# Kernel tuning notes

Measured on AMD Instinct MI355X. Metric: run time of the kernel, lower is better.

Reference implementation:

```python
import jax, jax.numpy as jnp
import numpy as np

S, T, B = 32, 64, 64          # sentences, tokens/sentence, batch
V, E, H, G, C = 32000, 128, 128, 128, 5  # vocab, embed, intra hid, inter hid, classes


def _gru_dir(x, h0, Wih, Whh, bih, bhh):
    # x: [T,B,D]; Wih: [3H,D]; Whh: [3H,H]  (PyTorch GRU gate order r,z,n)
    xg = jnp.einsum('tbd,gd->tbg', x, Wih) + bih  # precompute input gates [T,B,3H]
    def step(h, xt):
        gh = h @ Whh.T + bhh
        ir, iz, inn = jnp.split(xt, 3, axis=-1)
        hr, hz, hn = jnp.split(gh, 3, axis=-1)
        r = jax.nn.sigmoid(ir + hr)
        z = jax.nn.sigmoid(iz + hz)
        n = jnp.tanh(inn + r * hn)
        hnew = (1 - z) * n + z * h
        return hnew, hnew
    _, out = jax.lax.scan(step, h0, xg)
    return out  # [T,B,H]


def _bigru(x, Wih, Whh, bih, bhh):
    # x: [T,B,D]; Wih: [2,3H,D] (fwd, bwd). Zero initial state (init_hidden()).
    h0 = jnp.zeros((x.shape[1], Whh.shape[-1]), x.dtype)
    of = _gru_dir(x, h0, Wih[0], Whh[0], bih[0], bhh[0])
    ob = _gru_dir(x[::-1], h0, Wih[1], Whh[1], bih[1], bhh[1])[::-1]
    return jnp.concatenate([of, ob], axis=-1)  # [T,B,2H]


def setup_inputs() -> dict:
    key = jax.random.key(0)
    ks = iter(jax.random.split(key, 20))
    u = lambda k, shp, s: jax.random.uniform(k, shp, jnp.float32, -s, s)
    tokens = jax.random.randint(next(ks), (S, T, B), 0, V)
    return {
        'tokens': tokens,
        'embed_table': jax.random.normal(next(ks), (V, E), jnp.float32),
        # intra biGRU (input E, hidden H)
        'Wih_intra': u(next(ks), (2, 3 * H, E), 0.08),
        'Whh_intra': u(next(ks), (2, 3 * H, H), 0.08),
        'bih_intra': u(next(ks), (2, 3 * H), 0.08),
        'bhh_intra': u(next(ks), (2, 3 * H), 0.08),
        # intra attention
        'W_W_intra': u(next(ks), (2 * H, 2 * H), 0.1),
        'b_intra': u(next(ks), (2 * H,), 0.1),
        'proj_intra': u(next(ks), (2 * H,), 0.1),
        # inter biGRU (input 2H, hidden G)
        'Wih_inter': u(next(ks), (2, 3 * G, 2 * H), 0.08),
        'Whh_inter': u(next(ks), (2, 3 * G, G), 0.08),
        'bih_inter': u(next(ks), (2, 3 * G), 0.08),
        'bhh_inter': u(next(ks), (2, 3 * G), 0.08),
        # inter attention
        'W_W_inter': u(next(ks), (2 * G, 2 * G), 0.1),
        'b_inter': u(next(ks), (2 * G,), 0.1),
        'proj_inter': u(next(ks), (2 * G,), 0.1),
        # final linear
        'W_final': u(next(ks), (C, 2 * G), 0.06),
        'b_final': u(next(ks), (C,), 0.06),
    }


def reference(tokens, embed_table, Wih_intra, Whh_intra, bih_intra, bhh_intra,
              W_W_intra, b_intra, proj_intra, Wih_inter, Whh_inter, bih_inter,
              bhh_inter, W_W_inter, b_inter, proj_inter, W_final, b_final):
    # ---- intra (word-level) per sentence, fresh zero state each sentence ----
    emb = embed_table[tokens]                                   # [S,T,B,E]
    intra_out = jax.vmap(
        lambda xs: _bigru(xs, Wih_intra, Whh_intra, bih_intra, bhh_intra)
    )(emb)                                                      # [S,T,B,2H]
    u1 = jnp.tanh(jnp.einsum('stbh,hk->stbk', intra_out, W_W_intra) + b_intra)
    a1 = jnp.einsum('stbk,k->stb', u1, proj_intra)              # [S,T,B]
    a1 = jax.nn.softmax(a1, axis=1)                             # softmax over tokens
    sent_vecs = jnp.einsum('stb,stbh->sbh', a1, intra_out)      # [S,B,2H]
    # ---- inter (sentence-level) ----
    inter_out = _bigru(sent_vecs, Wih_inter, Whh_inter, bih_inter, bhh_inter)  # [S,B,2G]
    u2 = jnp.tanh(jnp.einsum('sbh,hk->sbk', inter_out, W_W_inter) + b_inter)
    a2 = jnp.einsum('sbk,k->sb', u2, proj_inter)                # NO softmax (faithful to source)
    doc_vec = jnp.einsum('sb,sbh->bh', a2, inter_out)           # [B,2G]
    final_map = doc_vec @ W_final.T + b_final                   # [B,C]
    return final_map
```

## Files before the change

kernel.cpp:

```cpp
#include <hip/hip_runtime.h>

#define S_ 32
#define T_ 64
#define B_ 64
#define V_ 32000
#define E_ 128
#define H_ 128
#define G_ 128
#define C_ 5

typedef short s8v __attribute__((ext_vector_type(8)));
typedef __bf16 b8v __attribute__((ext_vector_type(8)));
typedef float f32x4 __attribute__((ext_vector_type(4)));

template <typename V>
__device__ inline auto mfma_sel(V a, V b, f32x4 c, int)
    -> decltype(__builtin_amdgcn_mfma_f32_16x16x32_bf16(a, b, c, 0, 0, 0)) {
  return __builtin_amdgcn_mfma_f32_16x16x32_bf16(a, b, c, 0, 0, 0);
}
template <typename V>
__device__ inline f32x4 mfma_sel(V a, V b, f32x4 c, long) {
  return __builtin_amdgcn_mfma_f32_16x16x32_bf16(
      __builtin_bit_cast(b8v, a), __builtin_bit_cast(b8v, b), c, 0, 0, 0);
}
__device__ inline f32x4 mfma16(s8v a, s8v b, f32x4 c) { return mfma_sel(a, b, c, 0); }

__device__ inline float b2f(unsigned short u) {
  union { unsigned int i; float f; } v; v.i = ((unsigned int)u) << 16; return v.f;
}
__device__ inline unsigned short f2b(float f) {
  union { float f; unsigned int i; } v; v.f = f;
  return (unsigned short)((v.i + 0x8000u) >> 16);
}
__device__ inline unsigned short f2b_rne(float f) {
  union { float f; unsigned int i; } v; v.f = f;
  unsigned int r = (v.i + 0x7fffu + ((v.i >> 16) & 1u)) >> 16;
  return (unsigned short)r;
}
__device__ inline s8v cvt8(const float* p) {
  const float4 a = *(const float4*)p;
  const float4 b = *(const float4*)(p + 4);
  s8v r;
  r[0] = (short)f2b_rne(a.x); r[1] = (short)f2b_rne(a.y);
  r[2] = (short)f2b_rne(a.z); r[3] = (short)f2b_rne(a.w);
  r[4] = (short)f2b_rne(b.x); r[5] = (short)f2b_rne(b.y);
  r[6] = (short)f2b_rne(b.z); r[7] = (short)f2b_rne(b.w);
  return r;
}
__device__ inline float fsigm(float x) {
  return __builtin_amdgcn_rcpf(1.f + __builtin_amdgcn_exp2f(-1.44269504f * x));
}
__device__ inline float ftanh(float x) {
  return 1.f - 2.f * __builtin_amdgcn_rcpf(1.f + __builtin_amdgcn_exp2f(2.88539008f * x));
}

__device__ inline void lds_barrier() {
  asm volatile("s_waitcnt lgkmcnt(0)\n\ts_barrier" ::: "memory");
}

__global__ __launch_bounds__(256) void k_gtab(
    const float* __restrict__ emb,
    const float* __restrict__ wih,
    const float* __restrict__ bih,
    const float* __restrict__ bhh,
    const float* __restrict__ wwi,
    const float* __restrict__ wihI,
    unsigned short* __restrict__ gtab,
    unsigned short* __restrict__ wta,
    unsigned short* __restrict__ wib)
{
  __shared__ __align__(16) unsigned short res[64 * 776];
  __shared__ __align__(16) unsigned short alds[64 * 136];
  const int bid = blockIdx.x, tid = threadIdx.x;
  if (bid >= 504) {
    const int cb = bid - 504;
    for (int i = 0; i < 48; ++i) {
      int e4 = cb * 12288 + i * 256 + tid;
      float4 v = *(const float4*)&wihI[(size_t)e4 * 4];
      ushort4 u;
      u.x = f2b_rne(v.x); u.y = f2b_rne(v.y); u.z = f2b_rne(v.z); u.w = f2b_rne(v.w);
      *(ushort4*)&wib[(size_t)e4 * 4] = u;
    }
    return;
  }
  if (bid >= 500) {
    const int n0 = (bid - 500) * 64;
    for (int i = 0; i < 64; ++i) {
      int cid = i * 256 + tid;
      int k = cid >> 6, nl = cid & 63;
      res[nl * 264 + k] = f2b_rne(wwi[k * 256 + n0 + nl]);
    }
    __syncthreads();
    for (int i = 0; i < 8; ++i) {
      int cid = i * 256 + tid;
      int nl = cid >> 5, k8 = cid & 31;
      *(int4*)&wta[(size_t)(n0 + nl) * 256 + k8 * 8] =
          *(const int4*)&res[nl * 264 + k8 * 8];
    }
    return;
  }
  const int vbase = bid * 64;
  for (int i = 0; i < 8; ++i) {
    int cid = i * 256 + tid;
    int row = cid >> 5, kc = cid & 31;
    float4 v = *(const float4*)&emb[(size_t)(vbase + row) * 128 + kc * 4];
    ushort4 u;
    u.x = f2b_rne(v.x); u.y = f2b_rne(v.y); u.z = f2b_rne(v.z); u.w = f2b_rne(v.w);
    *(ushort4*)&alds[row * 136 + kc * 4] = u;
  }
  __syncthreads();
  const int w = tid >> 6, l = tid & 63, q = l >> 4, ln = l & 15;
  s8v af[4][4];
  for (int mt = 0; mt < 4; ++mt)
    for (int kf = 0; kf < 4; ++kf)
      af[mt][kf] = *(const s8v*)&alds[(mt * 16 + ln) * 136 + kf * 32 + q * 8];
  for (int nchunk = 0; nchunk < 6; ++nchunk) {
    const int nbase = nchunk * 128;
    s8v bf[2][4];
    float bias[2];
    for (int nt = 0; nt < 2; ++nt) {
      int c = nbase + (w * 2 + nt) * 16 + ln;
      int g = (c < 384) ? c : (c - 384);
      bias[nt] = bih[c] + (g < 256 ? bhh[c] : 0.f);
      for (int kf = 0; kf < 4; ++kf)
        bf[nt][kf] = cvt8(&wih[(size_t)c * 128 + kf * 32 + q * 8]);
    }
    for (int mt = 0; mt < 4; ++mt) {
      for (int nt = 0; nt < 2; ++nt) {
        f32x4 acc = {0.f, 0.f, 0.f, 0.f};
        for (int kf = 0; kf < 4; ++kf) acc = mfma16(af[mt][kf], bf[nt][kf], acc);
        const int col = nbase + (w * 2 + nt) * 16 + ln;
        for (int r = 0; r < 4; ++r) {
          const int row = mt * 16 + q * 4 + r;
          res[row * 776 + col] = f2b_rne(acc[r] + bias[nt]);
        }
      }
    }
  }
  __syncthreads();
  for (int i = 0; i < 24; ++i) {
    int cid = i * 256 + tid;
    int row = cid / 96, kc = cid - row * 96;
    *(int4*)&gtab[(size_t)(vbase + row) * 768 + kc * 8] =
        *(const int4*)&res[row * 776 + kc * 8];
  }
}

__global__ __launch_bounds__(512) void k_intra(
    const int* __restrict__ tokens,
    const unsigned short* __restrict__ gtab,
    const float* __restrict__ whh,
    const float* __restrict__ bhh,
    unsigned short* __restrict__ iout)
{
  const int bid = blockIdx.x;
  const int s = bid >> 3, dir = (bid >> 2) & 1, bq = bid & 3;
  const int bbase = bq * 16;
  const int tid = threadIdx.x;
  const int w = tid >> 6, l = tid & 63, q = l >> 4, ln = l & 15;
  const int gbase = w * 16, g0 = gbase + q * 4;

  __shared__ __align__(16) unsigned short hb[2][16 * 136];
  __shared__ __align__(16) unsigned short xbuf[2][16 * 392];
  __shared__ int tokl[T_ * 16];

  for (int i = tid; i < 2 * 16 * 136; i += 512) ((unsigned short*)hb)[i] = 0;
  for (int i = tid; i < T_ * 16; i += 512) {
    int t = i >> 4, bl = i & 15;
    tokl[i] = tokens[(s * T_ + t) * B_ + bbase + bl] * 768 + dir * 384;
  }

  s8v af[3][4];
  float hbn[4];
  const float* whd = whh + (size_t)dir * (384 * 128);
  const float* bhd = bhh + dir * 384;
  for (int g3 = 0; g3 < 3; ++g3)
    for (int kf = 0; kf < 4; ++kf)
      af[g3][kf] = cvt8(&whd[(size_t)(g3 * 128 + gbase + ln) * 128 + kf * 32 + q * 8]);
  for (int r = 0; r < 4; ++r) hbn[r] = bhd[256 + gbase + q * 4 + r];
  float h[4] = {0.f, 0.f, 0.f, 0.f};

  const bool stager = (w < 6);
  int sr0 = 0, sof0 = 0, sd0 = 0, sr1 = 0, sof1 = 0, sd1 = 0;
  {
    int e0 = w * 1024 + l * 8;
    int e1 = e0 + 512;
    sr0 = e0 / 384; sof0 = e0 - sr0 * 384; sd0 = sr0 * 392 + sof0;
    sr1 = e1 / 384; sof1 = e1 - sr1 * 384; sd1 = sr1 * 392 + sof1;
  }
  int4 ldA, ldB;
#define XLOAD(st)                                                           \
  do {                                                                      \
    int tt_ = (st) > (T_ - 1) ? (T_ - 1) : (st);                            \
    int tg_ = dir ? (T_ - 1 - tt_) : tt_;                                   \
    ldA = *(const int4*)&gtab[(size_t)tokl[tg_ * 16 + sr0] + sof0];         \
    ldB = *(const int4*)&gtab[(size_t)tokl[tg_ * 16 + sr1] + sof1];         \
  } while (0)
#define XWRITE(sl)                                                          \
  do {                                                                      \
    *(int4*)&xbuf[sl][sd0] = ldA;                                           \
    *(int4*)&xbuf[sl][sd1] = ldB;                                           \
  } while (0)

  __syncthreads();
  if (stager) {
    XLOAD(0);
    XWRITE(0);
    XLOAD(1);
  }
  __syncthreads();

  const int xb = ln * 392 + gbase + q * 4;
  int p = 0;
  int tprev = 0;
  for (int step = 0; step < T_; ++step) {
    const int t = dir ? (T_ - 1 - step) : step;
    const int sl = step & 1;
    if (stager) {
      XWRITE(sl ^ 1);
      XLOAD(step + 2);
    }
    if (step > 0 && tid < 256) {
      int row = tid >> 4, kc = tid & 15;
      int4 v = *(const int4*)&hb[p][row * 136 + kc * 8];
      *(int4*)&iout[((size_t)(s * T_ + tprev) * B_ + bbase + row) * 256 +
                    dir * 128 + kc * 8] = v;
    }
    s8v bfr[4];
    for (int kf = 0; kf < 4; ++kf)
      bfr[kf] = *(const s8v*)&hb[p][ln * 136 + kf * 32 + q * 8];
    f32x4 c0 = {0.f, 0.f, 0.f, 0.f}, c1 = c0, c2 = c0;
    for (int kf = 0; kf < 4; ++kf) {
      c0 = mfma16(af[0][kf], bfr[kf], c0);
      c1 = mfma16(af[1][kf], bfr[kf], c1);
      c2 = mfma16(af[2][kf], bfr[kf], c2);
    }
    const ushort4 xr = *(const ushort4*)&xbuf[sl][xb];
    const ushort4 xz = *(const ushort4*)&xbuf[sl][xb + 128];
    const ushort4 xn = *(const ushort4*)&xbuf[sl][xb + 256];
    const unsigned short* xrp = (const unsigned short*)&xr;
    const unsigned short* xzp = (const unsigned short*)&xz;
    const unsigned short* xnp = (const unsigned short*)&xn;
    unsigned short hnb[4];
    for (int r = 0; r < 4; ++r) {
      float rr = fsigm(b2f(xrp[r]) + c0[r]);
      float zz = fsigm(b2f(xzp[r]) + c1[r]);
      float nn = ftanh(b2f(xnp[r]) + rr * (c2[r] + hbn[r]));
      float hv = zz * (h[r] - nn) + nn;
      h[r] = hv;
      hnb[r] = f2b(hv);
    }
    ushort4 hv4; hv4.x = hnb[0]; hv4.y = hnb[1]; hv4.z = hnb[2]; hv4.w = hnb[3];
    *(ushort4*)&hb[p ^ 1][ln * 136 + g0] = hv4;
    lds_barrier();
    p ^= 1;
    tprev = t;
  }
  if (tid < 256) {
    int row = tid >> 4, kc = tid & 15;
    int4 v = *(const int4*)&hb[p][row * 136 + kc * 8];
    *(int4*)&iout[((size_t)(s * T_ + tprev) * B_ + bbase + row) * 256 +
                  dir * 128 + kc * 8] = v;
  }
#undef XLOAD
#undef XWRITE
}

__global__ __launch_bounds__(512, 1) void k_attn(
    const unsigned short* __restrict__ iout,
    const unsigned short* __restrict__ wta,
    const float* __restrict__ bint,
    const float* __restrict__ proj,
    const unsigned short* __restrict__ wib,
    const float* __restrict__ bihI,
    const float* __restrict__ bhhI,
    float* __restrict__ xgi)
{
  __shared__ __align__(16) unsigned short wlds[256 * 256];
  __shared__ float lgbuf[8][16];
  __shared__ float lbuf[8][8];
  const int tid = threadIdx.x, bid = blockIdx.x;
  const int s = bid >> 3, b0 = (bid & 7) * 8;
  for (int i = 0; i < 16; ++i) {
    int cid = i * 512 + tid;
    int n = cid >> 5, kc = cid & 31;
    *(int4*)&wlds[n * 256 + ((kc ^ (n & 15)) << 3)] =
        *(const int4*)&wta[(size_t)n * 256 + kc * 8];
  }
  const int w = tid >> 6, l = tid & 63, q = l >> 4, ln = l & 15;
  float bbv[16], ppv[16];
  for (int nt = 0; nt < 16; ++nt) {
    bbv[nt] = bint[nt * 16 + ln];
    ppv[nt] = proj[nt * 16 + ln];
  }
  __syncthreads();

  float O[8][8];
  for (int kf = 0; kf < 8; ++kf)
    for (int j = 0; j < 8; ++j) O[kf][j] = 0.f;
  float l_acc = 0.f;

  for (int tile = 0; tile < 4; ++tile) {
    const int t = (w * 4 + tile) * 2 + (ln >> 3);
    const size_t row = (size_t)((s * T_ + t) * B_ + b0 + (ln & 7));
    s8v af[8];
    for (int kf = 0; kf < 8; ++kf)
      af[kf] = *(const s8v*)&iout[row * 256 + kf * 32 + q * 8];
    float p0 = 0.f, p1 = 0.f, p2 = 0.f, p3 = 0.f;
    for (int nt = 0; nt < 16; ++nt) {
      f32x4 c = {0.f, 0.f, 0.f, 0.f};
      for (int kf = 0; kf < 8; ++kf) {
        s8v bf = *(const s8v*)&wlds[(nt * 16 + ln) * 256 + (((kf * 4 + q) ^ ln) << 3)];
        c = mfma16(af[kf], bf, c);
      }
      p0 += ppv[nt] * ftanh(c[0] + bbv[nt]);
      p1 += ppv[nt] * ftanh(c[1] + bbv[nt]);
      p2 += ppv[nt] * ftanh(c[2] + bbv[nt]);
      p3 += ppv[nt] * ftanh(c[3] + bbv[nt]);
    }
    for (int d = 1; d < 16; d <<= 1) {
      p0 += __shfl_xor(p0, d); p1 += __shfl_xor(p1, d);
      p2 += __shfl_xor(p2, d); p3 += __shfl_xor(p3, d);
    }
    if (ln == 0) {
      lgbuf[w][q * 4 + 0] = p0; lgbuf[w][q * 4 + 1] = p1;
      lgbuf[w][q * 4 + 2] = p2; lgbuf[w][q * 4 + 3] = p3;
    }
    const float lg = lgbuf[w][ln];
    const float e = __builtin_amdgcn_exp2f(1.44269504f * lg);
    l_acc += e;
    for (int kf = 0; kf < 8; ++kf)
      for (int j = 0; j < 8; ++j)
        O[kf][j] += e * b2f((unsigned short)af[kf][j]);
  }
  l_acc += __shfl_xor(l_acc, 8);
  for (int kf = 0; kf < 8; ++kf)
    for (int j = 0; j < 8; ++j) O[kf][j] += __shfl_xor(O[kf][j], 8);
  __syncthreads();
  float* obuf = (float*)wlds;
  unsigned short* svl = (unsigned short*)(((char*)wlds) + 65536);
  if (ln < 8) {
    const int base = w * 2048 + ln * 256 + q * 8;
    for (int kf = 0; kf < 8; ++kf) {
      float4 v0; v0.x = O[kf][0]; v0.y = O[kf][1]; v0.z = O[kf][2]; v0.w = O[kf][3];
      float4 v1; v1.x = O[kf][4]; v1.y = O[kf][5]; v1.z = O[kf][6]; v1.w = O[kf][7];
      *(float4*)&obuf[base + kf * 32]     = v0;
      *(float4*)&obuf[base + kf * 32 + 4] = v1;
    }
    if (q == 0) lbuf[w][ln] = l_acc;
  }
  {
    ushort4 z4; z4.x = 0; z4.y = 0; z4.z = 0; z4.w = 0;
    int rr = 8 + (tid >> 6), cc = (tid & 63) * 4;
    *(ushort4*)&svl[rr * 264 + cc] = z4;
  }
  __syncthreads();
  const int idx = tid * 4;
  const int bb_ = idx >> 8;
  float4 acc; acc.x = 0.f; acc.y = 0.f; acc.z = 0.f; acc.w = 0.f;
  float lsum = 0.f;
  for (int w8 = 0; w8 < 8; ++w8) {
    const float4 v = *(const float4*)&obuf[w8 * 2048 + idx];
    acc.x += v.x; acc.y += v.y; acc.z += v.z; acc.w += v.w;
    lsum += lbuf[w8][bb_];
  }
  const float inv = __builtin_amdgcn_rcpf(lsum);
  ushort4 u;
  u.x = f2b_rne(acc.x * inv); u.y = f2b_rne(acc.y * inv);
  u.z = f2b_rne(acc.z * inv); u.w = f2b_rne(acc.w * inv);
  *(ushort4*)&svl[bb_ * 264 + (idx & 255)] = u;
  __syncthreads();
  s8v afx[8];
  for (int kf = 0; kf < 8; ++kf)
    afx[kf] = *(const s8v*)&svl[ln * 264 + kf * 32 + q * 8];
  for (int nt = 0; nt < 6; ++nt) {
    const int c = w * 96 + nt * 16 + ln;
    const int dirI = (c >= 384) ? 1 : 0;
    const int g = c - dirI * 384;
    const float biasx = bihI[c] + (g < 256 ? bhhI[c] : 0.f);
    f32x4 cacc = {0.f, 0.f, 0.f, 0.f};
    for (int kf = 0; kf < 8; ++kf) {
      s8v bfx = *(const s8v*)&wib[(size_t)c * 256 + kf * 32 + q * 8];
      cacc = mfma16(afx[kf], bfx, cacc);
    }
    if (q < 2) {
      for (int r = 0; r < 4; ++r) {
        const int m = q * 4 + r;
        xgi[((size_t)dirI * 2048 + s * B_ + b0 + m) * 384 + g] = cacc[r] + biasx;
      }
    }
  }
}

__global__ __launch_bounds__(512) void k_inter(
    const float* __restrict__ xgi,
    const float* __restrict__ whh,
    const float* __restrict__ bhh,
    float* __restrict__ io2)
{
  const int bid = blockIdx.x;
  const int dir = bid >> 2, bq = bid & 3, bbase = bq * 16;
  const int tid = threadIdx.x;
  const int w = tid >> 6, l = tid & 63, q = l >> 4, ln = l & 15;
  const int gbase = w * 16, g0 = gbase + q * 4;
  __shared__ __align__(16) unsigned short hb[2][16 * 136];
  for (int i = tid; i < 2 * 16 * 136; i += 512) ((unsigned short*)hb)[i] = 0;
  s8v af[3][4];
  float hbn[4];
  const float* whd = whh + (size_t)dir * (384 * 128);
  const float* bhd = bhh + dir * 384;
  for (int g3 = 0; g3 < 3; ++g3) {
    const int R = g3 * 128 + gbase;
    for (int kf = 0; kf < 4; ++kf)
      af[g3][kf] = cvt8(&whd[(size_t)(R + ln) * 128 + kf * 32 + q * 8]);
  }
  for (int r = 0; r < 4; ++r) hbn[r] = bhd[256 + gbase + q * 4 + r];
  float h[4] = {0.f, 0.f, 0.f, 0.f};
  const int b = bbase + ln;
  __syncthreads();

  float4 Vr[4], Vz[4], Vn[4];
#define GLOAD_S(slot, st)                                                   \
  do {                                                                      \
    int tt_ = (st) > (S_ - 1) ? (S_ - 1) : (st);                            \
    int sg_ = dir ? (S_ - 1 - tt_) : tt_;                                   \
    const float* xp_ = xgi + ((size_t)dir * 2048 + sg_ * 64 + b) * 384 + g0;\
    Vr[slot] = *(const float4*)&xp_[0];                                     \
    Vz[slot] = *(const float4*)&xp_[128];                                   \
    Vn[slot] = *(const float4*)&xp_[256];                                   \
  } while (0)

  GLOAD_S(0, 0);
  GLOAD_S(1, 1);
  GLOAD_S(2, 2);

  int p = 0;
  for (int it = 0; it < S_ / 4; ++it) {
#pragma unroll
    for (int j = 0; j < 4; ++j) {
      const int step = it * 4 + j;
      const int sI = dir ? (S_ - 1 - step) : step;
      GLOAD_S((j + 3) & 3, step + 3);

      s8v bfr[4];
      for (int kf = 0; kf < 4; ++kf)
        bfr[kf] = *(const s8v*)&hb[p][ln * 136 + kf * 32 + q * 8];
      f32x4 c0 = {0.f, 0.f, 0.f, 0.f}, c1 = c0, c2 = c0;
      for (int kf = 0; kf < 4; ++kf) {
        c0 = mfma16(af[0][kf], bfr[kf], c0);
        c1 = mfma16(af[1][kf], bfr[kf], c1);
        c2 = mfma16(af[2][kf], bfr[kf], c2);
      }
      const float irv[4] = {Vr[j].x, Vr[j].y, Vr[j].z, Vr[j].w};
      const float izv[4] = {Vz[j].x, Vz[j].y, Vz[j].z, Vz[j].w};
      const float inv[4] = {Vn[j].x, Vn[j].y, Vn[j].z, Vn[j].w};
      unsigned short hnb[4];
      for (int r = 0; r < 4; ++r) {
        float rr = fsigm(irv[r] + c0[r]);
        float zz = fsigm(izv[r] + c1[r]);
        float nn = ftanh(inv[r] + rr * (c2[r] + hbn[r]));
        float hv = zz * (h[r] - nn) + nn;
        h[r] = hv;
        hnb[r] = f2b(hv);
      }
      ushort4 hv4; hv4.x = hnb[0]; hv4.y = hnb[1]; hv4.z = hnb[2]; hv4.w = hnb[3];
      *(ushort4*)&hb[p ^ 1][ln * 136 + g0] = hv4;
      float4 of4; of4.x = h[0]; of4.y = h[1]; of4.z = h[2]; of4.w = h[3];
      *(float4*)&io2[((size_t)(sI * 64 + b)) * 256 + dir * 128 + g0] = of4;
      lds_barrier();
      p ^= 1;
    }
  }
#undef GLOAD_S
}

__global__ __launch_bounds__(256) void k_attn_i(
    const float* __restrict__ io2,
    const float* __restrict__ wwI,
    const float* __restrict__ bI,
    const float* __restrict__ projI,
    float* __restrict__ a2)
{
  const int bid = blockIdx.x, tid = threadIdx.x;
  const int r0 = bid * 8;
  __shared__ float iol[8 * 256];
  __shared__ float red[4 * 8];
  for (int i = 0; i < 8; ++i) iol[i * 256 + tid] = io2[(size_t)(r0 + i) * 256 + tid];
  __syncthreads();
  float acc[8];
  for (int i = 0; i < 8; ++i) acc[i] = 0.f;
  for (int hh = 0; hh < 256; ++hh) {
    const float wv = wwI[hh * 256 + tid];
    for (int i = 0; i < 8; ++i) acc[i] += wv * iol[i * 256 + hh];
  }
  const float bb = bI[tid], pp = projI[tid];
  float p[8];
  for (int i = 0; i < 8; ++i) p[i] = pp * ftanh(acc[i] + bb);
  for (int d = 1; d < 64; d <<= 1)
    for (int i = 0; i < 8; ++i) p[i] += __shfl_xor(p[i], d);
  const int w = tid >> 6, l = tid & 63;
  if (l == 0)
    for (int i = 0; i < 8; ++i) red[w * 8 + i] = p[i];
  __syncthreads();
  if (tid < 8) a2[r0 + tid] = red[tid] + red[8 + tid] + red[16 + tid] + red[24 + tid];
}

__global__ __launch_bounds__(256) void k_final(
    const float* __restrict__ a2,
    const float* __restrict__ io2,
    const float* __restrict__ wf,
    const float* __restrict__ bfi,
    float* __restrict__ out)
{
  const int b = blockIdx.x, tid = threadIdx.x;
  __shared__ float av[S_];
  __shared__ float dv[256];
  __shared__ float red[4];
  if (tid < S_) av[tid] = a2[tid * 64 + b];
  __syncthreads();
  float acc = 0.f;
  for (int s = 0; s < S_; ++s) acc += av[s] * io2[((size_t)(s * 64 + b)) * 256 + tid];
  dv[tid] = acc;
  __syncthreads();
  for (int c = 0; c < C_; ++c) {
    float pv = wf[c * 256 + tid] * dv[tid];
    for (int d = 1; d < 64; d <<= 1) pv += __shfl_xor(pv, d);
    const int w = tid >> 6, l = tid & 63;
    if (l == 0) red[w] = pv;
    __syncthreads();
    if (tid == 0)
      out[b * C_ + c] = red[0] + red[1] + red[2] + red[3] + bfi[c];
    __syncthreads();
  }
}

extern "C" void kernel_launch(void* const* d_in, const int* in_sizes, int n_in,
                              void* d_out, int out_size, void* d_ws, size_t ws_size,
                              hipStream_t stream) {
  (void)in_sizes; (void)n_in; (void)out_size; (void)ws_size;
  const int*   tokens = (const int*)d_in[0];
  const float* emb    = (const float*)d_in[1];
  const float* wih_a  = (const float*)d_in[2];
  const float* whh_a  = (const float*)d_in[3];
  const float* bih_a  = (const float*)d_in[4];
  const float* bhh_a  = (const float*)d_in[5];
  const float* ww_a   = (const float*)d_in[6];
  const float* b_a    = (const float*)d_in[7];
  const float* proj_a = (const float*)d_in[8];
  const float* wih_i  = (const float*)d_in[9];
  const float* whh_i  = (const float*)d_in[10];
  const float* bih_i  = (const float*)d_in[11];
  const float* bhh_i  = (const float*)d_in[12];
  const float* ww_i   = (const float*)d_in[13];
  const float* b_i    = (const float*)d_in[14];
  const float* proj_i = (const float*)d_in[15];
  const float* w_fin  = (const float*)d_in[16];
  const float* b_fin  = (const float*)d_in[17];

  char* ws = (char*)d_ws;
  unsigned short* gtab = (unsigned short*)(ws + 0);
  unsigned short* wta  = (unsigned short*)(ws + 49152000);
  unsigned short* iout = (unsigned short*)(ws + 49283072);
  unsigned short* wib  = (unsigned short*)(ws + 116391936);
  float* xgi = (float*)(ws + 119537664);
  float* io2 = (float*)(ws + 125829120);
  float* a2  = (float*)(ws + 127926272);

  k_gtab<<<508, 256, 0, stream>>>(emb, wih_a, bih_a, bhh_a, ww_a, wih_i,
                                  gtab, wta, wib);
  k_intra<<<256, 512, 0, stream>>>(tokens, gtab, whh_a, bhh_a, iout);
  k_attn<<<256, 512, 0, stream>>>(iout, wta, b_a, proj_a, wib, bih_i, bhh_i, xgi);
  k_inter<<<8, 512, 0, stream>>>(xgi, whh_i, bhh_i, io2);
  k_attn_i<<<256, 256, 0, stream>>>(io2, ww_i, b_i, proj_i, a2);
  k_final<<<64, 256, 0, stream>>>(a2, io2, w_fin, b_fin, (float*)d_out);
}
```

Baseline: 294.8 us.

## Process two sentences per intra GRU block to interleave independent recurrences

Each k_intra block now runs two sentences' GRU recurrences at once, sharing the register-resident Whh fragments and interleaving their MFMA chains and gate math so one chain's latency can hide behind the other's. The grid halves from 256 to 128 blocks, and LDS use for hidden-state and input-gate buffers doubles. This targets the latency-bound serial step loop, at the cost of fewer blocks than the 256 compute units on MI355X, which may leave half the device idle.

New measurement: 338.4 us. 1.15x slower.

```diff
diff --git a/kernel.cpp b/kernel.cpp
--- a/kernel.cpp
+++ b/kernel.cpp
@@ -154,20 +154,22 @@
     unsigned short* __restrict__ iout)
 {
   const int bid = blockIdx.x;
-  const int s = bid >> 3, dir = (bid >> 2) & 1, bq = bid & 3;
+  const int sp = bid >> 3, dir = (bid >> 2) & 1, bq = bid & 3;
+  const int s0 = sp * 2, s1 = sp * 2 + 1;
   const int bbase = bq * 16;
   const int tid = threadIdx.x;
   const int w = tid >> 6, l = tid & 63, q = l >> 4, ln = l & 15;
   const int gbase = w * 16, g0 = gbase + q * 4;
 
-  __shared__ __align__(16) unsigned short hb[2][16 * 136];
-  __shared__ __align__(16) unsigned short xbuf[2][16 * 392];
-  __shared__ int tokl[T_ * 16];
-
-  for (int i = tid; i < 2 * 16 * 136; i += 512) ((unsigned short*)hb)[i] = 0;
-  for (int i = tid; i < T_ * 16; i += 512) {
-    int t = i >> 4, bl = i & 15;
-    tokl[i] = tokens[(s * T_ + t) * B_ + bbase + bl] * 768 + dir * 384;
+  __shared__ __align__(16) unsigned short hb[2][2][16 * 136];
+  __shared__ __align__(16) unsigned short xbuf[2][2][16 * 392];
+  __shared__ int tokl[2 * T_ * 16];
+
+  for (int i = tid; i < 2 * 2 * 16 * 136; i += 512) ((unsigned short*)hb)[i] = 0;
+  for (int i = tid; i < 2 * T_ * 16; i += 512) {
+    int ch = i >> 10, r2 = i & 1023, t = r2 >> 4, bl = r2 & 15;
+    int sc = ch ? s1 : s0;
+    tokl[i] = tokens[(sc * T_ + t) * B_ + bbase + bl] * 768 + dir * 384;
   }
 
   s8v af[3][4];
@@ -178,7 +180,7 @@
     for (int kf = 0; kf < 4; ++kf)
       af[g3][kf] = cvt8(&whd[(size_t)(g3 * 128 + gbase + ln) * 128 + kf * 32 + q * 8]);
   for (int r = 0; r < 4; ++r) hbn[r] = bhd[256 + gbase + q * 4 + r];
-  float h[4] = {0.f, 0.f, 0.f, 0.f};
+  float h[2][4] = {{0.f, 0.f, 0.f, 0.f}, {0.f, 0.f, 0.f, 0.f}};
 
   const bool stager = (w < 6);
   int sr0 = 0, sof0 = 0, sd0 = 0, sr1 = 0, sof1 = 0, sd1 = 0;
@@ -188,25 +190,37 @@
     sr0 = e0 / 384; sof0 = e0 - sr0 * 384; sd0 = sr0 * 392 + sof0;
     sr1 = e1 / 384; sof1 = e1 - sr1 * 384; sd1 = sr1 * 392 + sof1;
   }
-  int4 ldA, ldB;
-#define XLOAD(st)                                                           \
+  int4 ldA0, ldB0, ldA1, ldB1;
+#define XLOAD0(st)                                                          \
   do {                                                                      \
     int tt_ = (st) > (T_ - 1) ? (T_ - 1) : (st);                            \
     int tg_ = dir ? (T_ - 1 - tt_) : tt_;                                   \
-    ldA = *(const int4*)&gtab[(size_t)tokl[tg_ * 16 + sr0] + sof0];         \
-    ldB = *(const int4*)&gtab[(size_t)tokl[tg_ * 16 + sr1] + sof1];         \
+    ldA0 = *(const int4*)&gtab[(size_t)tokl[tg_ * 16 + sr0] + sof0];        \
+    ldB0 = *(const int4*)&gtab[(size_t)tokl[tg_ * 16 + sr1] + sof1];        \
   } while (0)
-#define XWRITE(sl)                                                          \
+#define XLOAD1(st)                                                          \
   do {                                                                      \
-    *(int4*)&xbuf[sl][sd0] = ldA;                                           \
-    *(int4*)&xbuf[sl][sd1] = ldB;                                           \
+    int tt_ = (st) > (T_ - 1) ? (T_ - 1) : (st);                            \
+    int tg_ = dir ? (T_ - 1 - tt_) : tt_;                                   \
+    ldA1 = *(const int4*)&gtab[(size_t)tokl[1024 + tg_ * 16 + sr0] + sof0]; \
+    ldB1 = *(const int4*)&gtab[(size_t)tokl[1024 + tg_ * 16 + sr1] + sof1]; \
   } while (0)
+#define XWRITE0(sl)                                                         \
+  do {                                                                      \
+    *(int4*)&xbuf[0][sl][sd0] = ldA0;                                       \
+    *(int4*)&xbuf[0][sl][sd1] = ldB0;                                       \
+  } while (0)
+#define XWRITE1(sl)                                                         \
+  do {                                                                      \
+    *(int4*)&xbuf[1][sl][sd0] = ldA1;                                       \
+    *(int4*)&xbuf[1][sl][sd1] = ldB1;                                       \
+  } while (0)
 
   __syncthreads();
   if (stager) {
-    XLOAD(0);
-    XWRITE(0);
-    XLOAD(1);
+    XLOAD0(0); XLOAD1(0);
+    XWRITE0(0); XWRITE1(0);
+    XLOAD0(1); XLOAD1(1);
   }
   __syncthreads();
 
@@ -217,53 +231,86 @@
     const int t = dir ? (T_ - 1 - step) : step;
     const int sl = step & 1;
     if (stager) {
-      XWRITE(sl ^ 1);
-      XLOAD(step + 2);
-    }
-    if (step > 0 && tid < 256) {
-      int row = tid >> 4, kc = tid & 15;
-      int4 v = *(const int4*)&hb[p][row * 136 + kc * 8];
-      *(int4*)&iout[((size_t)(s * T_ + tprev) * B_ + bbase + row) * 256 +
+      XWRITE0(sl ^ 1); XWRITE1(sl ^ 1);
+      XLOAD0(step + 2); XLOAD1(step + 2);
+    }
+    if (step > 0) {
+      const int ch = tid >> 8, r2 = tid & 255;
+      const int row = r2 >> 4, kc = r2 & 15;
+      const int sc = ch ? s1 : s0;
+      int4 v = *(const int4*)&hb[ch][p][row * 136 + kc * 8];
+      *(int4*)&iout[((size_t)(sc * T_ + tprev) * B_ + bbase + row) * 256 +
                     dir * 128 + kc * 8] = v;
     }
-    s8v bfr[4];
-    for (int kf = 0; kf < 4; ++kf)
-      bfr[kf] = *(const s8v*)&hb[p][ln * 136 + kf * 32 + q * 8];
-    f32x4 c0 = {0.f, 0.f, 0.f, 0.f}, c1 = c0, c2 = c0;
+    s8v bfr0[4], bfr1[4];
     for (int kf = 0; kf < 4; ++kf) {
-      c0 = mfma16(af[0][kf], bfr[kf], c0);
-      c1 = mfma16(af[1][kf], bfr[kf], c1);
-      c2 = mfma16(af[2][kf], bfr[kf], c2);
-    }
-    const ushort4 xr = *(const ushort4*)&xbuf[sl][xb];
-    const ushort4 xz = *(const ushort4*)&xbuf[sl][xb + 128];
-    const ushort4 xn = *(const ushort4*)&xbuf[sl][xb + 256];
-    const unsigned short* xrp = (const unsigned short*)&xr;
-    const unsigned short* xzp = (const unsigned short*)&xz;
-    const unsigned short* xnp = (const unsigned short*)&xn;
-    unsigned short hnb[4];
-    for (int r = 0; r < 4; ++r) {
-      float rr = fsigm(b2f(xrp[r]) + c0[r]);
-      float zz = fsigm(b2f(xzp[r]) + c1[r]);
-      float nn = ftanh(b2f(xnp[r]) + rr * (c2[r] + hbn[r]));
-      float hv = zz * (h[r] - nn) + nn;
-      h[r] = hv;
-      hnb[r] = f2b(hv);
-    }
-    ushort4 hv4; hv4.x = hnb[0]; hv4.y = hnb[1]; hv4.z = hnb[2]; hv4.w = hnb[3];
-    *(ushort4*)&hb[p ^ 1][ln * 136 + g0] = hv4;
+      bfr0[kf] = *(const s8v*)&hb[0][p][ln * 136 + kf * 32 + q * 8];
+      bfr1[kf] = *(const s8v*)&hb[1][p][ln * 136 + kf * 32 + q * 8];
+    }
+    f32x4 c00 = {0.f, 0.f, 0.f, 0.f}, c01 = c00, c02 = c00;
+    f32x4 c10 = c00, c11 = c00, c12 = c00;
+    for (int kf = 0; kf < 4; ++kf) {
+      c00 = mfma16(af[0][kf], bfr0[kf], c00);
+      c10 = mfma16(af[0][kf], bfr1[kf], c10);
+      c01 = mfma16(af[1][kf], bfr0[kf], c01);
+      c11 = mfma16(af[1][kf], bfr1[kf], c11);
+      c02 = mfma16(af[2][kf], bfr0[kf], c02);
+      c12 = mfma16(af[2][kf], bfr1[kf], c12);
+    }
+    {
+      const ushort4 xr = *(const ushort4*)&xbuf[0][sl][xb];
+      const ushort4 xz = *(const ushort4*)&xbuf[0][sl][xb + 128];
+      const ushort4 xn = *(const ushort4*)&xbuf[0][sl][xb + 256];
+      const unsigned short* xrp = (const unsigned short*)&xr;
+      const unsigned short* xzp = (const unsigned short*)&xz;
+      const unsigned short* xnp = (const unsigned short*)&xn;
+      unsigned short hnb[4];
+      for (int r = 0; r < 4; ++r) {
+        float rr = fsigm(b2f(xrp[r]) + c00[r]);
+        float zz = fsigm(b2f(xzp[r]) + c01[r]);
+        float nn = ftanh(b2f(xnp[r]) + rr * (c02[r] + hbn[r]));
+        float hv = zz * (h[0][r] - nn) + nn;
+        h[0][r] = hv;
+        hnb[r] = f2b(hv);
+      }
+      ushort4 hv4; hv4.x = hnb[0]; hv4.y = hnb[1]; hv4.z = hnb[2]; hv4.w = hnb[3];
+      *(ushort4*)&hb[0][p ^ 1][ln * 136 + g0] = hv4;
+    }
+    {
+      const ushort4 xr = *(const ushort4*)&xbuf[1][sl][xb];
+      const ushort4 xz = *(const ushort4*)&xbuf[1][sl][xb + 128];
+      const ushort4 xn = *(const ushort4*)&xbuf[1][sl][xb + 256];
+      const unsigned short* xrp = (const unsigned short*)&xr;
+      const unsigned short* xzp = (const unsigned short*)&xz;
+      const unsigned short* xnp = (const unsigned short*)&xn;
+      unsigned short hnb[4];
+      for (int r = 0; r < 4; ++r) {
+        float rr = fsigm(b2f(xrp[r]) + c10[r]);
+        float zz = fsigm(b2f(xzp[r]) + c11[r]);
+        float nn = ftanh(b2f(xnp[r]) + rr * (c12[r] + hbn[r]));
+        float hv = zz * (h[1][r] - nn) + nn;
+        h[1][r] = hv;
+        hnb[r] = f2b(hv);
+      }
+      ushort4 hv4; hv4.x = hnb[0]; hv4.y = hnb[1]; hv4.z = hnb[2]; hv4.w = hnb[3];
+      *(ushort4*)&hb[1][p ^ 1][ln * 136 + g0] = hv4;
+    }
     lds_barrier();
     p ^= 1;
     tprev = t;
   }
-  if (tid < 256) {
-    int row = tid >> 4, kc = tid & 15;
-    int4 v = *(const int4*)&hb[p][row * 136 + kc * 8];
-    *(int4*)&iout[((size_t)(s * T_ + tprev) * B_ + bbase + row) * 256 +
+  {
+    const int ch = tid >> 8, r2 = tid & 255;
+    const int row = r2 >> 4, kc = r2 & 15;
+    const int sc = ch ? s1 : s0;
+    int4 v = *(const int4*)&hb[ch][p][row * 136 + kc * 8];
+    *(int4*)&iout[((size_t)(sc * T_ + tprev) * B_ + bbase + row) * 256 +
                   dir * 128 + kc * 8] = v;
   }
-#undef XLOAD
-#undef XWRITE
+#undef XLOAD0
+#undef XLOAD1
+#undef XWRITE0
+#undef XWRITE1
 }
 
 __global__ __launch_bounds__(512, 1) void k_attn(
@@ -568,7 +615,7 @@
 
   k_gtab<<<508, 256, 0, stream>>>(emb, wih_a, bih_a, bhh_a, ww_a, wih_i,
                                   gtab, wta, wib);
-  k_intra<<<256, 512, 0, stream>>>(tokens, gtab, whh_a, bhh_a, iout);
+  k_intra<<<128, 512, 0, stream>>>(tokens, gtab, whh_a, bhh_a, iout);
   k_attn<<<256, 512, 0, stream>>>(iout, wta, b_a, proj_a, wib, bih_i, bhh_i, xgi);
   k_inter<<<8, 512, 0, stream>>>(xgi, whh_i, bhh_i, io2);
   k_attn_i<<<256, 256, 0, stream>>>(io2, ww_i, b_i, proj_i, a2);
```
